# Kernel optimization log

Hardware: AMD Instinct MI355X
Metric: run time of the kernel (lower is better)

The kernel has to match this reference:

```python
import jax, jax.numpy as jnp
import numpy as np

B, C, H, W = 256, 1024, 7, 7
D_HID, N_CLS = 768, 5

def setup_inputs() -> dict:
    key = jax.random.key(0)
    k1, k2, k3, k4, k5 = jax.random.split(key, 5)
    flat = C * H * W  # 50176
    return {
        "features": jax.random.normal(k1, (B, C, H, W), dtype=jnp.float32),
        "W1": jax.random.normal(k2, (D_HID, flat), dtype=jnp.float32) * 0.02,
        "b1": jax.random.normal(k3, (D_HID,), dtype=jnp.float32) * 0.02,
        "W2": jax.random.normal(k4, (N_CLS, D_HID), dtype=jnp.float32) * 0.02,
        "b2": jax.random.normal(k5, (N_CLS,), dtype=jnp.float32) * 0.02,
    }

def reference(features, W1, b1, W2, b2):
    # PCAM: per-(batch, channel) global max over spatial dims, broadcast-multiplied
    # back onto the feature map. Replaces the torch Python double loop with one
    # fused reduce-max + elementwise multiply.
    ch_max = jnp.max(features, axis=(2, 3), keepdims=True)  # [B, C, 1, 1]
    pcams = features * ch_max                               # [B, C, H, W]
    flat = pcams.reshape(pcams.shape[0], -1)                # [B, C*H*W]
    h = jax.nn.relu(flat @ W1.T + b1)                       # [B, 768]
    logits = h @ W2.T + b2                                  # [B, num_classes]
    return (logits, features)
```

## Files before the change

kernel.cpp:

```cpp
#include <hip/hip_runtime.h>
#include <hip/hip_bf16.h>

#define B_SZ   256
#define C_SZ   1024
#define HW     49
#define KDIM   50176
#define DHID   768
#define NCLS   5

typedef __bf16 bf16x8 __attribute__((ext_vector_type(8)));
typedef __bf16 bf16x4 __attribute__((ext_vector_type(4)));
typedef float  f32x4  __attribute__((ext_vector_type(4)));

#define GLOAD_LDS16(gsrc, ldst) \
  __builtin_amdgcn_global_load_lds((__attribute__((address_space(1))) void*)(gsrc), \
                                   (__attribute__((address_space(3))) void*)(ldst), 16, 0, 0)

#define FENCE()   asm volatile("" ::: "memory")
#define BARRIER() do { \
    asm volatile("s_waitcnt lgkmcnt(0)" ::: "memory"); \
    __builtin_amdgcn_s_barrier(); \
    asm volatile("" ::: "memory"); \
  } while (0)

__global__ __launch_bounds__(256) void pcam_kernel(const float* __restrict__ feat,
                                                   float* __restrict__ feat_out,
                                                   __bf16* __restrict__ pcam) {
  __shared__ float sv[1568];
  __shared__ float smax[32];
  const int tid = threadIdx.x;
  const size_t base = (size_t)blockIdx.x * 1568;

  const float4* src4 = (const float4*)(feat + base);
  float4* dst4 = (float4*)(feat_out + base);
  #pragma unroll
  for (int i = 0; i < 2; ++i) {
    int idx = tid + i * 256;
    if (idx < 392) {
      float4 v = src4[idx];
      dst4[idx] = v;
      ((float4*)sv)[idx] = v;
    }
  }
  __syncthreads();

  {
    const int r = tid >> 3, p = tid & 7;
    float mx = -INFINITY;
    for (int i = p; i < HW; i += 8) mx = fmaxf(mx, sv[r * HW + i]);
    #pragma unroll
    for (int off = 1; off < 8; off <<= 1) mx = fmaxf(mx, __shfl_xor(mx, off));
    if (p == 0) smax[r] = mx;
  }
  __syncthreads();

  for (int i = tid; i < 1568; i += 256) {
    int r = (i * 1338) >> 16;
    float v = sv[i] * smax[r];
    pcam[base + i] = (__bf16)v;
  }
}

#define BM 256
#define BN 256
#define BK 64
#define NT 3
#define KSPLIT 85
#define KSTEPS 784

__global__ __launch_bounds__(512, 1) void gemm1_kernel(const __bf16* __restrict__ pcam,
                                                       const float* __restrict__ W1,
                                                       __bf16* __restrict__ h_part) {
  __shared__ __bf16 Asm[2][BM * BK];
  __shared__ __bf16 Bsm[2][BN * BK];

  const int tid  = threadIdx.x;
  const int lane = tid & 63;
  const int w    = tid >> 6;
  const int c_   = lane & 15;
  const int q_   = lane >> 4;
  const int n0   = blockIdx.x * BN;
  const int ks   = blockIdx.y;
  const int s0   = (ks * KSTEPS) / KSPLIT;
  const int s1   = ((ks + 1) * KSTEPS) / KSPLIT;

  unsigned a_off[4];
  #pragma unroll
  for (int it = 0; it < 4; ++it) {
    const unsigned ug = it * 512 + tid;
    const unsigned m  = ug >> 3;
    a_off[it] = m * (unsigned)KDIM + (((ug & 7) ^ (m & 7)) * 8u);
  }

  const float* bbase = W1 + (size_t)(n0 + w * 32 + q_) * KDIM + c_ * 4;
  int bwr[8];
  #pragma unroll
  for (int i = 0; i < 8; ++i) {
    const int r = w * 32 + i * 4 + q_;
    bwr[i] = r * 128 + (((c_ >> 1) ^ (r & 7)) << 4) + ((c_ & 1) << 3);
  }

  f32x4 acc[16][2];
  #pragma unroll
  for (int i = 0; i < 16; ++i)
    #pragma unroll
    for (int j = 0; j < 2; ++j) acc[i][j] = f32x4{0.f, 0.f, 0.f, 0.f};

  f32x4 pA0, pA1, pA2, pA3, pA4, pA5, pA6, pA7;
  f32x4 pB0, pB1, pB2, pB3, pB4, pB5, pB6, pB7;

#define ISSUE_B8(Q0,Q1,Q2,Q3,Q4,Q5,Q6,Q7, s) do { \
    const size_t kb = (size_t)(s) * BK; \
    Q0 = *(const f32x4*)(bbase + kb + (size_t)( 0) * KDIM); \
    Q1 = *(const f32x4*)(bbase + kb + (size_t)( 4) * KDIM); \
    Q2 = *(const f32x4*)(bbase + kb + (size_t)( 8) * KDIM); \
    Q3 = *(const f32x4*)(bbase + kb + (size_t)(12) * KDIM); \
    Q4 = *(const f32x4*)(bbase + kb + (size_t)(16) * KDIM); \
    Q5 = *(const f32x4*)(bbase + kb + (size_t)(20) * KDIM); \
    Q6 = *(const f32x4*)(bbase + kb + (size_t)(24) * KDIM); \
    Q7 = *(const f32x4*)(bbase + kb + (size_t)(28) * KDIM); \
    FENCE(); \
  } while (0)

#define ISSUE_A(bi, s) do { \
    const unsigned ka = (unsigned)(s) * BK; \
    _Pragma("unroll") \
    for (int it = 0; it < 4; ++it) \
      GLOAD_LDS16(pcam + a_off[it] + ka, (char*)Asm[bi] + it * 8192 + w * 1024); \
    FENCE(); \
  } while (0)

#define WRITE_B8(bi, Q0,Q1,Q2,Q3,Q4,Q5,Q6,Q7) do { \
    _Pragma("unroll") \
    for (int i = 0; i < 8; ++i) { \
      const f32x4 v = (i==0)?Q0:(i==1)?Q1:(i==2)?Q2:(i==3)?Q3:(i==4)?Q4:(i==5)?Q5:(i==6)?Q6:Q7; \
      bf16x4 bv; \
      bv[0] = (__bf16)v[0]; bv[1] = (__bf16)v[1]; \
      bv[2] = (__bf16)v[2]; bv[3] = (__bf16)v[3]; \
      *(bf16x4*)((char*)Bsm[bi] + bwr[i]) = bv; \
    } \
  } while (0)

#define COMPUTE(bi) do { \
    _Pragma("unroll") \
    for (int ksub = 0; ksub < 2; ++ksub) { \
      const int u = ksub * 4 + q_; \
      bf16x8 bfr[2]; \
      _Pragma("unroll") \
      for (int j = 0; j < 2; ++j) { \
        const int rn = w * 32 + j * 16 + c_; \
        bfr[j] = *(const bf16x8*)((const char*)Bsm[bi] + rn * 128 + ((u ^ (rn & 7)) << 4)); \
      } \
      _Pragma("unroll") \
      for (int i = 0; i < 16; ++i) { \
        const int m = i * 16 + c_; \
        const bf16x8 af = *(const bf16x8*)((const char*)Asm[bi] + m * 128 + ((u ^ (m & 7)) << 4)); \
        acc[i][0] = __builtin_amdgcn_mfma_f32_16x16x32_bf16(af, bfr[0], acc[i][0], 0, 0, 0); \
        acc[i][1] = __builtin_amdgcn_mfma_f32_16x16x32_bf16(af, bfr[1], acc[i][1], 0, 0, 0); \
      } \
    } \
  } while (0)

  ISSUE_B8(pA0,pA1,pA2,pA3,pA4,pA5,pA6,pA7, s0);
  ISSUE_A(0, s0);
  if (s0 + 1 < s1) {
    ISSUE_B8(pB0,pB1,pB2,pB3,pB4,pB5,pB6,pB7, s0 + 1);
    asm volatile("s_waitcnt vmcnt(8)" ::: "memory");
  } else {
    asm volatile("s_waitcnt vmcnt(0)" ::: "memory");
  }
  WRITE_B8(0, pA0,pA1,pA2,pA3,pA4,pA5,pA6,pA7);
  BARRIER();
  if (s0 + 1 < s1) ISSUE_A(1, s0 + 1);

  for (int s = s0; s < s1; ++s) {
    const int cur = (s - s0) & 1;
    if (s + 2 < s1) {
      if (cur == 0) ISSUE_B8(pA0,pA1,pA2,pA3,pA4,pA5,pA6,pA7, s + 2);
      else          ISSUE_B8(pB0,pB1,pB2,pB3,pB4,pB5,pB6,pB7, s + 2);
    }
    COMPUTE(cur);
    if (s + 1 < s1) {
      if (s + 2 < s1) asm volatile("s_waitcnt vmcnt(8)" ::: "memory");
      else            asm volatile("s_waitcnt vmcnt(0)" ::: "memory");
      if (cur == 0) WRITE_B8(1, pB0,pB1,pB2,pB3,pB4,pB5,pB6,pB7);
      else          WRITE_B8(0, pA0,pA1,pA2,pA3,pA4,pA5,pA6,pA7);
      BARRIER();
      if (s + 2 < s1) ISSUE_A(cur, s + 2);
    }
  }

  __bf16* out = h_part + (size_t)ks * DHID * B_SZ;
  #pragma unroll
  for (int j = 0; j < 2; ++j) {
    const int n = n0 + w * 32 + j * 16 + c_;
    #pragma unroll
    for (int i = 0; i < 16; ++i) {
      const int mb = i * 16 + q_ * 4;
      bf16x4 pv;
      pv[0] = (__bf16)acc[i][j][0]; pv[1] = (__bf16)acc[i][j][1];
      pv[2] = (__bf16)acc[i][j][2]; pv[3] = (__bf16)acc[i][j][3];
      *(bf16x4*)(out + (size_t)n * B_SZ + mb) = pv;
    }
  }
#undef ISSUE_B8
#undef ISSUE_A
#undef WRITE_B8
#undef COMPUTE
}

__global__ __launch_bounds__(256) void reduce_kernel(const __bf16* __restrict__ h_part,
                                                     const float* __restrict__ b1,
                                                     float* __restrict__ h) {
  const int n = blockIdx.x;
  const int m = threadIdx.x;
  float s = 0.f;
  #pragma unroll 5
  for (int ks = 0; ks < KSPLIT; ++ks)
    s += (float)h_part[((size_t)ks * DHID + n) * B_SZ + m];
  float v = s + b1[n];
  h[(size_t)m * DHID + n] = v > 0.f ? v : 0.f;
}

__global__ __launch_bounds__(64) void head_kernel(const float* __restrict__ h,
                                                  const float* __restrict__ W2,
                                                  const float* __restrict__ b2,
                                                  float* __restrict__ logits) {
  const int m = blockIdx.x;
  const int lane = threadIdx.x;
  float hv[12];
  #pragma unroll
  for (int j = 0; j < 12; ++j) hv[j] = h[(size_t)m * DHID + j * 64 + lane];
  #pragma unroll
  for (int c = 0; c < NCLS; ++c) {
    float s = 0.f;
    #pragma unroll
    for (int j = 0; j < 12; ++j) s += hv[j] * W2[c * DHID + j * 64 + lane];
    #pragma unroll
    for (int off = 32; off > 0; off >>= 1) s += __shfl_xor(s, off);
    if (lane == 0) logits[m * NCLS + c] = s + b2[c];
  }
}

extern "C" void kernel_launch(void* const* d_in, const int* in_sizes, int n_in,
                              void* d_out, int out_size, void* d_ws, size_t ws_size,
                              hipStream_t stream) {
  const float* feat = (const float*)d_in[0];
  const float* W1   = (const float*)d_in[1];
  const float* b1   = (const float*)d_in[2];
  const float* W2   = (const float*)d_in[3];
  const float* b2   = (const float*)d_in[4];

  float* logits   = (float*)d_out;
  float* feat_out = (float*)d_out + (size_t)B_SZ * NCLS;

  char* ws = (char*)d_ws;
  __bf16* pcam   = (__bf16*)ws;
  __bf16* h_part = (__bf16*)(ws + (size_t)B_SZ * KDIM * 2);
  float*  h      = (float*)(ws + (size_t)B_SZ * KDIM * 2
                               + (size_t)KSPLIT * DHID * B_SZ * 2);

  pcam_kernel<<<(B_SZ * C_SZ) / 32, 256, 0, stream>>>(feat, feat_out, pcam);
  gemm1_kernel<<<dim3(NT, KSPLIT), 512, 0, stream>>>(pcam, W1, h_part);
  reduce_kernel<<<DHID, 256, 0, stream>>>(h_part, b1, h);
  head_kernel<<<B_SZ, 64, 0, stream>>>(h, W2, b2, logits);
}
```

Measured before the change: 95.97 us.

## Prepack W1 into bf16 MFMA fragment layout and feed B from registers

Adds a repack kernel that converts W1 from fp32 to bf16 on every call and stores it in a layout that matches the MFMA B-fragments. The GEMM then loads B fragments straight into registers with a triple-buffered rotation, removing the B shared-memory tile, its conversion writes and the related LDS traffic. The trade-off is an extra pass over W1 each call: one full fp32 read plus a bf16 write, before the GEMM reads it again. That may cost more memory bandwidth than the shared-memory work saves. The main loop now runs a fixed unrolled count, with clamped prefetch indices and guarded compute.

Result: slower. 127.4 us (+32.7%).

```diff
diff --git a/kernel.cpp b/kernel.cpp
--- a/kernel.cpp
+++ b/kernel.cpp
@@ -61,6 +61,45 @@
   }
 }
 
+__global__ __launch_bounds__(256) void repack_kernel(const float* __restrict__ W1,
+                                                     __bf16* __restrict__ Wp) {
+  __shared__ float ls[16 * 228];
+  const int tid = threadIdx.x;
+  const int f   = blockIdx.x >> 5;
+  const int ss  = blockIdx.x & 31;
+
+  for (int sub = 0; sub < 7; ++sub) {
+    const size_t k0 = (size_t)ss * 1568 + sub * 224;
+    #pragma unroll
+    for (int it = 0; it < 4; ++it) {
+      const int fi = it * 256 + tid;
+      if (fi < 896) {
+        const int row  = fi / 56;
+        const int col4 = fi % 56;
+        const float4 v = *(const float4*)(W1 + (size_t)(f * 16 + row) * KDIM + k0 + col4 * 4);
+        *(float4*)(ls + row * 228 + col4 * 4) = v;
+      }
+    }
+    __syncthreads();
+    #pragma unroll
+    for (int it = 0; it < 2; ++it) {
+      const int oi = it * 256 + tid;
+      if (oi < 448) {
+        const int rr  = oi & 15;
+        const int oct = (oi >> 4) & 3;
+        const int kcl = oi >> 6;
+        const float* src = ls + rr * 228 + kcl * 32 + oct * 8;
+        bf16x8 o;
+        #pragma unroll
+        for (int e = 0; e < 8; ++e) o[e] = (__bf16)src[e];
+        const size_t kc = (size_t)ss * 49 + sub * 7 + kcl;
+        *(bf16x8*)(Wp + (((size_t)f * 1568 + kc) * 64 + oct * 16 + rr) * 8) = o;
+      }
+    }
+    __syncthreads();
+  }
+}
+
 #define BM 256
 #define BN 256
 #define BK 64
@@ -69,17 +108,16 @@
 #define KSTEPS 784
 
 __global__ __launch_bounds__(512, 1) void gemm1_kernel(const __bf16* __restrict__ pcam,
-                                                       const float* __restrict__ W1,
+                                                       const __bf16* __restrict__ Wp,
                                                        __bf16* __restrict__ h_part) {
   __shared__ __bf16 Asm[2][BM * BK];
-  __shared__ __bf16 Bsm[2][BN * BK];
 
   const int tid  = threadIdx.x;
   const int lane = tid & 63;
   const int w    = tid >> 6;
   const int c_   = lane & 15;
   const int q_   = lane >> 4;
-  const int n0   = blockIdx.x * BN;
+  const int nt   = blockIdx.x;
   const int ks   = blockIdx.y;
   const int s0   = (ks * KSTEPS) / KSPLIT;
   const int s1   = ((ks + 1) * KSTEPS) / KSPLIT;
@@ -92,13 +130,8 @@
     a_off[it] = m * (unsigned)KDIM + (((ug & 7) ^ (m & 7)) * 8u);
   }
 
-  const float* bbase = W1 + (size_t)(n0 + w * 32 + q_) * KDIM + c_ * 4;
-  int bwr[8];
-  #pragma unroll
-  for (int i = 0; i < 8; ++i) {
-    const int r = w * 32 + i * 4 + q_;
-    bwr[i] = r * 128 + (((c_ >> 1) ^ (r & 7)) << 4) + ((c_ & 1) << 3);
-  }
+  const __bf16* pb0 = Wp + (size_t)(nt * 16 + w * 2 + 0) * 1568 * 512 + lane * 8;
+  const __bf16* pb1 = Wp + (size_t)(nt * 16 + w * 2 + 1) * 1568 * 512 + lane * 8;
 
   f32x4 acc[16][2];
   #pragma unroll
@@ -106,94 +139,72 @@
     #pragma unroll
     for (int j = 0; j < 2; ++j) acc[i][j] = f32x4{0.f, 0.f, 0.f, 0.f};
 
-  f32x4 pA0, pA1, pA2, pA3, pA4, pA5, pA6, pA7;
-  f32x4 pB0, pB1, pB2, pB3, pB4, pB5, pB6, pB7;
-
-#define ISSUE_B8(Q0,Q1,Q2,Q3,Q4,Q5,Q6,Q7, s) do { \
-    const size_t kb = (size_t)(s) * BK; \
-    Q0 = *(const f32x4*)(bbase + kb + (size_t)( 0) * KDIM); \
-    Q1 = *(const f32x4*)(bbase + kb + (size_t)( 4) * KDIM); \
-    Q2 = *(const f32x4*)(bbase + kb + (size_t)( 8) * KDIM); \
-    Q3 = *(const f32x4*)(bbase + kb + (size_t)(12) * KDIM); \
-    Q4 = *(const f32x4*)(bbase + kb + (size_t)(16) * KDIM); \
-    Q5 = *(const f32x4*)(bbase + kb + (size_t)(20) * KDIM); \
-    Q6 = *(const f32x4*)(bbase + kb + (size_t)(24) * KDIM); \
-    Q7 = *(const f32x4*)(bbase + kb + (size_t)(28) * KDIM); \
+  bf16x8 b0_0a, b0_0b, b0_1a, b0_1b;
+  bf16x8 b1_0a, b1_0b, b1_1a, b1_1b;
+  bf16x8 b2_0a, b2_0b, b2_1a, b2_1b;
+
+#define ISSUE_B(K0a, K0b, K1a, K1b, t) do { \
+    const size_t kb = (size_t)(t) * 2 * 512; \
+    K0a = *(const bf16x8*)(pb0 + kb); \
+    K0b = *(const bf16x8*)(pb1 + kb); \
+    K1a = *(const bf16x8*)(pb0 + kb + 512); \
+    K1b = *(const bf16x8*)(pb1 + kb + 512); \
     FENCE(); \
   } while (0)
 
-#define ISSUE_A(bi, s) do { \
-    const unsigned ka = (unsigned)(s) * BK; \
+#define ISSUE_A(par, t) do { \
+    const unsigned ka = (unsigned)(t) * BK; \
     _Pragma("unroll") \
     for (int it = 0; it < 4; ++it) \
-      GLOAD_LDS16(pcam + a_off[it] + ka, (char*)Asm[bi] + it * 8192 + w * 1024); \
+      GLOAD_LDS16(pcam + a_off[it] + ka, (char*)Asm[par] + it * 8192 + w * 1024); \
     FENCE(); \
   } while (0)
 
-#define WRITE_B8(bi, Q0,Q1,Q2,Q3,Q4,Q5,Q6,Q7) do { \
-    _Pragma("unroll") \
-    for (int i = 0; i < 8; ++i) { \
-      const f32x4 v = (i==0)?Q0:(i==1)?Q1:(i==2)?Q2:(i==3)?Q3:(i==4)?Q4:(i==5)?Q5:(i==6)?Q6:Q7; \
-      bf16x4 bv; \
-      bv[0] = (__bf16)v[0]; bv[1] = (__bf16)v[1]; \
-      bv[2] = (__bf16)v[2]; bv[3] = (__bf16)v[3]; \
-      *(bf16x4*)((char*)Bsm[bi] + bwr[i]) = bv; \
-    } \
-  } while (0)
-
-#define COMPUTE(bi) do { \
+#define COMPUTE(par, K0a, K0b, K1a, K1b) do { \
     _Pragma("unroll") \
     for (int ksub = 0; ksub < 2; ++ksub) { \
+      const bf16x8 f0 = ksub ? K1a : K0a; \
+      const bf16x8 f1 = ksub ? K1b : K0b; \
       const int u = ksub * 4 + q_; \
-      bf16x8 bfr[2]; \
-      _Pragma("unroll") \
-      for (int j = 0; j < 2; ++j) { \
-        const int rn = w * 32 + j * 16 + c_; \
-        bfr[j] = *(const bf16x8*)((const char*)Bsm[bi] + rn * 128 + ((u ^ (rn & 7)) << 4)); \
-      } \
       _Pragma("unroll") \
       for (int i = 0; i < 16; ++i) { \
         const int m = i * 16 + c_; \
-        const bf16x8 af = *(const bf16x8*)((const char*)Asm[bi] + m * 128 + ((u ^ (m & 7)) << 4)); \
-        acc[i][0] = __builtin_amdgcn_mfma_f32_16x16x32_bf16(af, bfr[0], acc[i][0], 0, 0, 0); \
-        acc[i][1] = __builtin_amdgcn_mfma_f32_16x16x32_bf16(af, bfr[1], acc[i][1], 0, 0, 0); \
+        const bf16x8 af = *(const bf16x8*)((const char*)Asm[par] + m * 128 + ((u ^ (m & 7)) << 4)); \
+        acc[i][0] = __builtin_amdgcn_mfma_f32_16x16x32_bf16(af, f0, acc[i][0], 0, 0, 0); \
+        acc[i][1] = __builtin_amdgcn_mfma_f32_16x16x32_bf16(af, f1, acc[i][1], 0, 0, 0); \
       } \
     } \
   } while (0)
 
-  ISSUE_B8(pA0,pA1,pA2,pA3,pA4,pA5,pA6,pA7, s0);
   ISSUE_A(0, s0);
-  if (s0 + 1 < s1) {
-    ISSUE_B8(pB0,pB1,pB2,pB3,pB4,pB5,pB6,pB7, s0 + 1);
-    asm volatile("s_waitcnt vmcnt(8)" ::: "memory");
-  } else {
-    asm volatile("s_waitcnt vmcnt(0)" ::: "memory");
-  }
-  WRITE_B8(0, pA0,pA1,pA2,pA3,pA4,pA5,pA6,pA7);
+  ISSUE_B(b0_0a, b0_0b, b0_1a, b0_1b, s0);
+  ISSUE_B(b1_0a, b1_0b, b1_1a, b1_1b, s0 + 1);
+  asm volatile("s_waitcnt vmcnt(4)" ::: "memory");
   BARRIER();
-  if (s0 + 1 < s1) ISSUE_A(1, s0 + 1);
-
-  for (int s = s0; s < s1; ++s) {
-    const int cur = (s - s0) & 1;
-    if (s + 2 < s1) {
-      if (cur == 0) ISSUE_B8(pA0,pA1,pA2,pA3,pA4,pA5,pA6,pA7, s + 2);
-      else          ISSUE_B8(pB0,pB1,pB2,pB3,pB4,pB5,pB6,pB7, s + 2);
-    }
-    COMPUTE(cur);
-    if (s + 1 < s1) {
-      if (s + 2 < s1) asm volatile("s_waitcnt vmcnt(8)" ::: "memory");
-      else            asm volatile("s_waitcnt vmcnt(0)" ::: "memory");
-      if (cur == 0) WRITE_B8(1, pB0,pB1,pB2,pB3,pB4,pB5,pB6,pB7);
-      else          WRITE_B8(0, pA0,pA1,pA2,pA3,pA4,pA5,pA6,pA7);
-      BARRIER();
-      if (s + 2 < s1) ISSUE_A(cur, s + 2);
-    }
-  }
+  ISSUE_A(1, s0 + 1);
+
+#define STEP(JI, CS0a, CS0b, CS1a, CS1b, IS0a, IS0b, IS1a, IS1b) do { \
+    const int r  = jo * 3 + (JI); \
+    const int t  = s0 + r; \
+    const int tc = (t + 2 < s1) ? (t + 2) : (s1 - 1); \
+    ISSUE_B(IS0a, IS0b, IS1a, IS1b, tc); \
+    if (t < s1) COMPUTE((r & 1), CS0a, CS0b, CS1a, CS1b); \
+    asm volatile("s_waitcnt vmcnt(4)" ::: "memory"); \
+    BARRIER(); \
+    ISSUE_A((r & 1), tc); \
+  } while (0)
+
+  for (int jo = 0; jo < 4; ++jo) {
+    STEP(0, b0_0a, b0_0b, b0_1a, b0_1b, b2_0a, b2_0b, b2_1a, b2_1b);
+    STEP(1, b1_0a, b1_0b, b1_1a, b1_1b, b0_0a, b0_0b, b0_1a, b0_1b);
+    STEP(2, b2_0a, b2_0b, b2_1a, b2_1b, b1_0a, b1_0b, b1_1a, b1_1b);
+  }
+#undef STEP
 
   __bf16* out = h_part + (size_t)ks * DHID * B_SZ;
   #pragma unroll
   for (int j = 0; j < 2; ++j) {
-    const int n = n0 + w * 32 + j * 16 + c_;
+    const int n = nt * BN + w * 32 + j * 16 + c_;
     #pragma unroll
     for (int i = 0; i < 16; ++i) {
       const int mb = i * 16 + q_ * 4;
@@ -203,9 +214,8 @@
       *(bf16x4*)(out + (size_t)n * B_SZ + mb) = pv;
     }
   }
-#undef ISSUE_B8
+#undef ISSUE_B
 #undef ISSUE_A
-#undef WRITE_B8
 #undef COMPUTE
 }
 
@@ -256,12 +266,13 @@
 
   char* ws = (char*)d_ws;
   __bf16* pcam   = (__bf16*)ws;
-  __bf16* h_part = (__bf16*)(ws + (size_t)B_SZ * KDIM * 2);
-  float*  h      = (float*)(ws + (size_t)B_SZ * KDIM * 2
-                               + (size_t)KSPLIT * DHID * B_SZ * 2);
+  __bf16* Wp     = (__bf16*)(ws + 25690112);
+  __bf16* h_part = (__bf16*)(ws + 25690112 + 77070336);
+  float*  h      = (float*) (ws + 25690112 + 77070336 + 33423360);
 
   pcam_kernel<<<(B_SZ * C_SZ) / 32, 256, 0, stream>>>(feat, feat_out, pcam);
-  gemm1_kernel<<<dim3(NT, KSPLIT), 512, 0, stream>>>(pcam, W1, h_part);
+  repack_kernel<<<48 * 32, 256, 0, stream>>>(W1, Wp);
+  gemm1_kernel<<<dim3(NT, KSPLIT), 512, 0, stream>>>(pcam, Wp, h_part);
   reduce_kernel<<<DHID, 256, 0, stream>>>(h_part, b1, h);
   head_kernel<<<B_SZ, 64, 0, stream>>>(h, W2, b2, logits);
 }
```
